# Kernel optimization log

Hardware: AMD Instinct MI355X
Metric: run time of the kernel (lower is better)

Reference implementation:

```python
import math
import jax, jax.numpy as jnp
import numpy as np


def _conv(x, w, b, stride, pad):
    y = jax.lax.conv_general_dilated(x, w, (stride, stride), [(pad, pad), (pad, pad)],
                                     dimension_numbers=('NCHW', 'OIHW', 'NCHW'))
    return y + b[None, :, None, None]


def _deconv(x, w, b):
    y = jax.lax.conv_transpose(x, w, (2, 2), 'SAME', dimension_numbers=('NCHW', 'HWIO', 'NCHW'))
    return y + b[None, :, None, None]


def _res_stack(h, w1, b1, w2, b2):
    for i in range(w1.shape[0]):  # small fixed num_residual_layers
        r = _conv(jax.nn.relu(h), w1[i], b1[i], 1, 1)
        r = _conv(jax.nn.relu(r), w2[i], b2[i], 1, 0)
        h = h + r
    return jax.nn.relu(h)


def _gcn_edges(x, w, b, src, dst):
    n = x.shape[0]
    xl = x @ w
    deg = 1.0 + jax.ops.segment_sum(jnp.ones_like(dst, dtype=xl.dtype), dst, num_segments=n)
    dinv = jax.lax.rsqrt(deg)
    coef = (dinv[src] * dinv[dst])[:, None]
    agg = jax.ops.segment_sum(xl[src] * coef, dst, num_segments=n)
    return agg + xl / deg[:, None] + b


def setup_inputs() -> dict:
    key = jax.random.key(0)
    ks = jax.random.split(key, 40)
    B, C, H, D, E, Hg, R, L, hid = 256, 3, 64, 256, 16, 64, 32, 2, 128
    f = H // 4
    flat = hid * f * f  # 32768

    def n(k, shape, s=0.02):
        return jax.random.normal(k, shape, jnp.float32) * s

    i = jnp.arange(B - 1)
    src = jnp.concatenate([i, i + 1])
    dst = jnp.concatenate([i + 1, i])
    inp = {
        'x': jax.random.normal(ks[0], (B, C, H, H), jnp.float32),
        'eps': jax.random.normal(ks[1], (B, D), jnp.float32),
        'edge_index': jnp.stack([src, dst]).astype(jnp.int32),
        'enc_conv1_w': n(ks[2], (hid // 2, C, 4, 4)), 'enc_conv1_b': n(ks[3], (hid // 2,)),
        'enc_conv2_w': n(ks[4], (hid, hid // 2, 4, 4)), 'enc_conv2_b': n(ks[5], (hid,)),
        'enc_conv3_w': n(ks[6], (hid, hid, 3, 3)), 'enc_conv3_b': n(ks[7], (hid,)),
        'enc_res_w1': n(ks[8], (L, R, hid, 3, 3)), 'enc_res_b1': n(ks[9], (L, R)),
        'enc_res_w2': n(ks[10], (L, hid, R, 1, 1)), 'enc_res_b2': n(ks[11], (L, hid)),
        'fc_mu_w': n(ks[12], (flat, D)), 'fc_mu_b': n(ks[13], (D,)),
        'fc_logvar_w': n(ks[14], (flat, D)), 'fc_logvar_b': n(ks[15], (D,)),
        'dec_fc_w': n(ks[16], (D, flat)), 'dec_fc_b': n(ks[17], (flat,)),
        'dec_res_w1': n(ks[18], (L, R, hid, 3, 3)), 'dec_res_b1': n(ks[19], (L, R)),
        'dec_res_w2': n(ks[20], (L, hid, R, 1, 1)), 'dec_res_b2': n(ks[21], (L, hid)),
        'dec_ct1_w': n(ks[22], (4, 4, hid, hid // 2)), 'dec_ct1_b': n(ks[23], (hid // 2,)),
        'dec_ct2_w': n(ks[24], (4, 4, hid // 2, C)), 'dec_ct2_b': n(ks[25], (C,)),
        'inst_w': n(ks[26], (2, D, D), 0.05), 'inst_b': n(ks[27], (2, D), 0.02),
        'dim_adj_logits': jax.random.normal(ks[28], (D, D), jnp.float32),
        'dim_embeddings': jax.random.normal(ks[29], (D, E), jnp.float32),
        'dg1_w': n(ks[30], (E, Hg), 0.2), 'dg1_b': n(ks[31], (Hg,), 0.02),
        'dg2_w': n(ks[32], (Hg, 1), 0.2), 'dg2_b': n(ks[33], (1,), 0.02),
    }
    return inp


def reference(x, eps, edge_index, enc_conv1_w, enc_conv1_b, enc_conv2_w, enc_conv2_b,
              enc_conv3_w, enc_conv3_b, enc_res_w1, enc_res_b1, enc_res_w2, enc_res_b2,
              fc_mu_w, fc_mu_b, fc_logvar_w, fc_logvar_b, dec_fc_w, dec_fc_b,
              dec_res_w1, dec_res_b1, dec_res_w2, dec_res_b2,
              dec_ct1_w, dec_ct1_b, dec_ct2_w, dec_ct2_b,
              inst_w, inst_b, dim_adj_logits, dim_embeddings, dg1_w, dg1_b, dg2_w, dg2_b):
    B = x.shape[0]
    D = dim_adj_logits.shape[0]
    # ---- encode ----
    h = jax.nn.relu(_conv(x, enc_conv1_w, enc_conv1_b, 2, 1))
    h = jax.nn.relu(_conv(h, enc_conv2_w, enc_conv2_b, 2, 1))
    h = _conv(h, enc_conv3_w, enc_conv3_b, 1, 1)
    h = _res_stack(h, enc_res_w1, enc_res_b1, enc_res_w2, enc_res_b2)
    flat = h.reshape(B, -1)
    mu = flat @ fc_mu_w + fc_mu_b
    logvar = flat @ fc_logvar_w + fc_logvar_b
    sigma = jnp.exp(0.5 * logvar)
    # ---- instance GNN over chain tree ----
    src, dst = edge_index[0], edge_index[1]
    v = mu
    for i in range(inst_w.shape[0]):
        v = jax.nn.relu(_gcn_edges(v, inst_w[i], inst_b[i], src, dst))
    v_inst = v
    # ---- dim GNN: thresholded dense adjacency, dense GCN (math-identical to edge-list GCNConv) ----
    eye = jnp.eye(D, dtype=x.dtype)
    logits = (dim_adj_logits + dim_adj_logits.T) * (1.0 - eye)
    mask = (jax.nn.sigmoid(logits) > 0.5).astype(x.dtype) * (1.0 - eye)
    mask = jnp.where(mask.sum() > 0, mask, 1.0 - eye)  # fallback: complete graph
    a_hat = mask + eye
    dinv = jax.lax.rsqrt(a_hat.sum(1))
    norm_adj = a_hat * dinv[:, None] * dinv[None, :]
    xd = jax.nn.relu(norm_adj @ (dim_embeddings @ dg1_w) + dg1_b)
    dim_importance = (norm_adj @ (xd @ dg2_w) + dg2_b)[:, 0]
    # ---- reparameterize + decode ----
    vv = v_inst * dim_importance[None, :]
    z = mu + sigma * (eps * vv)
    hd = (z @ dec_fc_w + dec_fc_b).reshape(B, enc_conv3_w.shape[0], x.shape[2] // 4, x.shape[3] // 4)
    hd = _res_stack(hd, dec_res_w1, dec_res_b1, dec_res_w2, dec_res_b2)
    hd = jax.nn.relu(_deconv(hd, dec_ct1_w, dec_ct1_b))
    recon = _deconv(hd, dec_ct2_w, dec_ct2_b)
    # ---- ELBO ----
    log_px_z = -jnp.sum((recon - x) ** 2)
    prior = -0.5 * jnp.sum(z ** 2 + math.log(2 * math.pi))
    entropy = 0.5 * jnp.sum(1.0 + jnp.log(sigma ** 2 + 1e-8))
    elbo = log_px_z + prior + entropy
    lv = jnp.log(sigma ** 2 + 1e-8)
    kl_per_dim = -0.5 * (1.0 + lv - mu ** 2 - jnp.exp(lv))
    num_active_dims = jnp.sum(kl_per_dim.mean(0) > 0.01)
    return recon, elbo, num_active_dims, dim_importance, v_inst
```

## Files before the change

### kernel.cpp

```cpp
#include <hip/hip_runtime.h>
#include <math.h>

#define OUT_ELBO  3145728
#define OUT_NACT  3145729
#define OUT_IMP   3145730
#define OUT_VINST 3145986

__device__ __forceinline__ float relu_(float v){ return fmaxf(v, 0.f); }

__device__ __forceinline__ unsigned short f2bf(float f){
  unsigned int u = __float_as_uint(f);
  unsigned int r = (u + 0x7FFFu + ((u>>16)&1u)) >> 16;
  return (unsigned short)r;
}

typedef __attribute__((ext_vector_type(8))) short short8;
typedef __attribute__((ext_vector_type(4))) float f32x4;

__global__ __launch_bounds__(512) void k_conv1(const float* __restrict__ in,
    const float* __restrict__ w, const float* __restrict__ bias, float* __restrict__ out){
  __shared__ float li[13068];
  __shared__ float lw[1536];
  int cohalf = blockIdx.x & 1;
  int n      = blockIdx.x >> 1;
  int co0 = cohalf*32;
  int tid = threadIdx.x;
  for (int i=tid; i<13068; i+=512) li[i] = 0.f;
  __syncthreads();
  const float* ip = in + (size_t)n*12288;
  for (int i=tid; i<12288; i+=512){
    int ci = i >> 12, rem = i & 4095;
    int yy = rem >> 6, xx = rem & 63;
    li[ci*4356 + (yy+1)*66 + xx+1] = ip[i];
  }
  for (int i=tid; i<1536; i+=512){
    int t = i >> 5, c = i & 31;
    lw[i] = w[(co0+c)*48 + t];
  }
  __syncthreads();
  int x = tid & 31, y8 = tid >> 5;
  #pragma unroll
  for (int cc=0; cc<4; cc++){
    float acc[2][8];
    #pragma unroll
    for (int q=0;q<2;q++)
      #pragma unroll
      for (int c=0;c<8;c++) acc[q][c]=0.f;
    #pragma unroll
    for (int ci=0; ci<3; ci++){
      int cb = ci*4356;
      #pragma unroll
      for (int ky=0; ky<4; ky++){
        float v[2][4];
        #pragma unroll
        for (int q=0;q<2;q++){
          int y = y8 + 16*q;
          int rb = cb + (2*y+ky)*66 + 2*x;
          v[q][0]=li[rb]; v[q][1]=li[rb+1]; v[q][2]=li[rb+2]; v[q][3]=li[rb+3];
        }
        float wv[4][8];
        #pragma unroll
        for (int kx=0;kx<4;kx++){
          int wb = ((ci*4+ky)*4+kx)*32 + cc*8;
          #pragma unroll
          for (int c=0;c<8;c++) wv[kx][c] = lw[wb+c];
        }
        #pragma unroll
        for (int q=0;q<2;q++)
          #pragma unroll
          for (int kx=0;kx<4;kx++)
            #pragma unroll
            for (int c=0;c<8;c++)
              acc[q][c] += v[q][kx]*wv[kx][c];
      }
    }
    #pragma unroll
    for (int c=0;c<8;c++){
      int co = co0 + cc*8 + c;
      float bv = bias[co];
      #pragma unroll
      for (int q=0;q<2;q++){
        int y = y8 + 16*q;
        out[(((size_t)n*64+co)*32 + y)*32 + x] = relu_(acc[q][c] + bv);
      }
    }
  }
}

__global__ __launch_bounds__(256) void k_wt2(const float* __restrict__ w,
    unsigned short* __restrict__ Wt){
  int idx = blockIdx.x*256 + threadIdx.x;
  int ci = idx & 63;
  int r = idx >> 6;
  int t = r >> 7, co = r & 127;
  Wt[idx] = f2bf(w[((co*64 + ci)<<4) + t]);
}

__global__ __launch_bounds__(256) void k_at2(const float* __restrict__ in,
    unsigned short* __restrict__ At){
  __shared__ unsigned int l[256*33];
  int n = blockIdx.x, tid = threadIdx.x;
  const float* ip = in + (size_t)n*65536;
  unsigned short* Ab = At + (size_t)n*1156*64;
  for (int c=0;c<4;c++){
    __syncthreads();
    int pxg = c*256 + tid;
    for (int j=0;j<64;j+=2){
      float a = ip[j*1024 + pxg];
      float b = ip[(j+1)*1024 + pxg];
      l[tid*33 + (j>>1)] = (unsigned int)f2bf(a) | ((unsigned int)f2bf(b)<<16);
    }
    __syncthreads();
    #pragma unroll
    for (int it=0; it<8; it++){
      int u = it*256 + tid;
      int pxl = u >> 3, seg = u & 7;
      int pxg2 = c*256 + pxl;
      int y = pxg2 >> 5, x = pxg2 & 31;
      int pp = (y+1)*34 + (x+1);
      uint4 v;
      v.x = l[pxl*33 + seg*4 + 0];
      v.y = l[pxl*33 + seg*4 + 1];
      v.z = l[pxl*33 + seg*4 + 2];
      v.w = l[pxl*33 + seg*4 + 3];
      *(uint4*)(Ab + pp*64 + seg*8) = v;
    }
  }
  uint4 z; z.x=0; z.y=0; z.z=0; z.w=0;
  for (int it=0; it<5; it++){
    int u = it*256 + tid;
    if (u >= 1056) break;
    int h = u >> 3, seg = u & 7;
    int pp;
    if (h < 34) pp = h;
    else if (h < 68) pp = 1122 + (h-34);
    else { int s = h-68; pp = (1 + (s>>1))*34 + (s&1)*33; }
    *(uint4*)(Ab + pp*64 + seg*8) = z;
  }
}

__global__ __launch_bounds__(256) void k_c2mfma(const unsigned short* __restrict__ At,
    const unsigned short* __restrict__ Wt, const float* __restrict__ bias,
    float* __restrict__ out){
  int b = blockIdx.x;
  int wsw = (b & 7)*32 + (b >> 3);
  int half = wsw & 1;
  int n    = wsw >> 1;
  int tid = threadIdx.x;
  int wid = tid >> 6, lane = tid & 63;
  int wn = wid & 1, wm = wid >> 1;
  int lrow = lane & 15, lkb = lane >> 4;
  f32x4 acc[4][4];
  #pragma unroll
  for (int i=0;i<4;i++)
    #pragma unroll
    for (int j=0;j<4;j++){ acc[i][j].x=0.f; acc[i][j].y=0.f; acc[i][j].z=0.f; acc[i][j].w=0.f; }
  const unsigned short* Ab = At + (size_t)n*1156*64;
  int mbase = half*128 + wm*64;
  #pragma unroll
  for (int t=0; t<16; t++){
    int ky = t >> 2, kx = t & 3;
    #pragma unroll
    for (int kc=0; kc<2; kc++){
      int k0 = kc*32 + lkb*8;
      short8 a[4], b2[4];
      #pragma unroll
      for (int i=0;i<4;i++){
        int m = mbase + i*16 + lrow;
        int y = m >> 4, x = m & 15;
        int pp = (2*y+ky)*34 + (2*x+kx);
        a[i] = *(const short8*)(Ab + pp*64 + k0);
      }
      #pragma unroll
      for (int j=0;j<4;j++){
        int co = wn*64 + j*16 + lrow;
        b2[j] = *(const short8*)(Wt + (t*128 + co)*64 + k0);
      }
      #pragma unroll
      for (int i=0;i<4;i++)
        #pragma unroll
        for (int j=0;j<4;j++)
          acc[i][j] = __builtin_amdgcn_mfma_f32_16x16x32_bf16(a[i], b2[j], acc[i][j], 0,0,0);
    }
  }
  #pragma unroll
  for (int j=0;j<4;j++){
    int co = wn*64 + j*16 + lrow;
    float bv = bias[co];
    #pragma unroll
    for (int i=0;i<4;i++){
      int px0 = mbase + i*16 + lkb*4;
      f32x4 v = acc[i][j];
      v.x = relu_(v.x + bv); v.y = relu_(v.y + bv);
      v.z = relu_(v.z + bv); v.w = relu_(v.w + bv);
      *(f32x4*)(out + ((size_t)n*128+co)*256 + px0) = v;
    }
  }
}

__global__ __launch_bounds__(256) void k_wt(const float* __restrict__ w,
    unsigned short* __restrict__ Wt, int Co){
  int idx = blockIdx.x*256 + threadIdx.x;
  int tot = Co*128*9;
  if (idx >= tot) return;
  int ci = idx & 127;
  int r = idx >> 7;
  int t = r / Co, co = r - t*Co;
  Wt[idx] = f2bf(w[(co*128 + ci)*9 + t]);
}

__global__ __launch_bounds__(256) void k_wt1(const float* __restrict__ w,
    unsigned short* __restrict__ Wt){
  int idx = blockIdx.x*256 + threadIdx.x;
  int ci = idx & 127;
  int r = idx >> 7;
  int t = r >> 6, co = r & 63;
  Wt[idx] = f2bf(w[t*8192 + ci*64 + co]);
}

__global__ __launch_bounds__(256) void k_at(const float* __restrict__ in,
    unsigned short* __restrict__ At, int relu){
  __shared__ unsigned int l[256*67];
  int n = blockIdx.x, tid = threadIdx.x;
  for (int j=0;j<128;j+=2){
    float a = in[(n*128+j  )*256 + tid];
    float b = in[(n*128+j+1)*256 + tid];
    if (relu){ a = relu_(a); b = relu_(b); }
    l[tid*67 + (j>>1)] = (unsigned int)f2bf(a) | ((unsigned int)f2bf(b)<<16);
  }
  __syncthreads();
  unsigned short* Ab = At + (size_t)n*324*128;
  #pragma unroll
  for (int it=0; it<16; it++){
    int u = it*256 + tid;
    int px = u >> 4, seg = u & 15;
    int y = px >> 4, x = px & 15;
    int pp = (y+1)*18 + (x+1);
    uint4 v;
    v.x = l[px*67 + seg*4 + 0];
    v.y = l[px*67 + seg*4 + 1];
    v.z = l[px*67 + seg*4 + 2];
    v.w = l[px*67 + seg*4 + 3];
    *(uint4*)(Ab + pp*128 + seg*8) = v;
  }
  uint4 z; z.x=0; z.y=0; z.z=0; z.w=0;
  for (int it=0; it<5; it++){
    int u = it*256 + tid;
    if (u >= 1088) break;
    int h = u >> 4, seg = u & 15;
    int pp;
    if (h < 18) pp = h;
    else if (h < 36) pp = 306 + (h-18);
    else { int s = h-36; pp = 18 + (s>>1)*18 + (s&1)*17; }
    *(uint4*)(Ab + pp*128 + seg*8) = z;
  }
}

template<int CO>
__global__ __launch_bounds__(512) void k_c3mfma(const unsigned short* __restrict__ At,
    const unsigned short* __restrict__ Wt, const float* __restrict__ bias,
    float* __restrict__ out){
  constexpr int WNW = (CO==128) ? 2 : 1;
  constexpr int WMW = 8/WNW;
  constexpr int MT  = 16/WMW;
  constexpr int NT  = (CO/16)/WNW;
  __shared__ short8 lA[16][324];
  int n = blockIdx.x;
  int tid = threadIdx.x;
  const short8* src = (const short8*)(At + (size_t)n*324*128);
  #pragma unroll
  for (int it=0; it<11; it++){
    int u = it*512 + tid;
    if (u < 5184) lA[u & 15][u >> 4] = src[u];
  }
  __syncthreads();
  int wid = tid >> 6, lane = tid & 63;
  int wn = wid % WNW, wm = wid / WNW;
  int lrow = lane & 15, lkb = lane >> 4;
  f32x4 acc[MT][NT];
  #pragma unroll
  for (int i=0;i<MT;i++)
    #pragma unroll
    for (int j=0;j<NT;j++){ acc[i][j].x=0.f; acc[i][j].y=0.f; acc[i][j].z=0.f; acc[i][j].w=0.f; }
  for (int t=0; t<9; t++){
    int ky = t/3, kx = t - 3*(t/3);
    #pragma unroll
    for (int kc=0; kc<4; kc++){
      int ch = kc*4 + lkb;
      int k0 = kc*32 + lkb*8;
      short8 a[MT], b[NT];
      #pragma unroll
      for (int i=0;i<MT;i++){
        int m = wm*(MT*16) + i*16 + lrow;
        int y = m >> 4, x = m & 15;
        int pp = (y+ky)*18 + (x+kx);
        a[i] = lA[ch][pp];
      }
      #pragma unroll
      for (int j=0;j<NT;j++){
        int co = wn*(NT*16) + j*16 + lrow;
        b[j] = *(const short8*)(Wt + (t*CO + co)*128 + k0);
      }
      #pragma unroll
      for (int i=0;i<MT;i++)
        #pragma unroll
        for (int j=0;j<NT;j++)
          acc[i][j] = __builtin_amdgcn_mfma_f32_16x16x32_bf16(a[i], b[j], acc[i][j], 0,0,0);
    }
  }
  #pragma unroll
  for (int j=0;j<NT;j++){
    int co = wn*(NT*16) + j*16 + lrow;
    float bv = bias[co];
    #pragma unroll
    for (int i=0;i<MT;i++){
      int px0 = wm*(MT*16) + i*16 + lkb*4;
      f32x4 v = acc[i][j];
      v.x += bv; v.y += bv; v.z += bv; v.w += bv;
      *(f32x4*)(out + ((size_t)n*CO+co)*256 + px0) = v;
    }
  }
}

__global__ __launch_bounds__(512) void k_dc1mfma(const unsigned short* __restrict__ At,
    const unsigned short* __restrict__ Wt, const float* __restrict__ bias,
    float* __restrict__ out){
  __shared__ short8 lA[16][324];
  int b = blockIdx.x;
  int wsw = (b & 7)*64 + (b >> 3);
  int half = wsw & 1;
  int n    = wsw >> 1;
  int tid = threadIdx.x;
  const short8* src = (const short8*)(At + (size_t)n*324*128);
  #pragma unroll
  for (int it=0; it<11; it++){
    int u = it*512 + tid;
    if (u < 5184) lA[u & 15][u >> 4] = src[u];
  }
  __syncthreads();
  int wid = tid >> 6, lane = tid & 63;
  int cls = half*2 + (wid >> 2);
  int wm  = wid & 3;
  int p_y = cls >> 1, p_x = cls & 1;
  int lrow = lane & 15, lkb = lane >> 4;
  f32x4 acc[4][4];
  #pragma unroll
  for (int i=0;i<4;i++)
    #pragma unroll
    for (int j=0;j<4;j++){ acc[i][j].x=0.f; acc[i][j].y=0.f; acc[i][j].z=0.f; acc[i][j].w=0.f; }
  #pragma unroll
  for (int kc=0; kc<16; kc++){
    int tapi = kc >> 2;
    int a = tapi >> 1, bb = tapi & 1;
    int ch = (kc & 3)*4 + lkb;
    int k0 = (kc & 3)*32 + lkb*8;
    int t = (p_y + 2*a)*4 + (p_x + 2*bb);
    short8 av[4], bv[4];
    #pragma unroll
    for (int i=0;i<4;i++){
      int m = wm*64 + i*16 + lrow;
      int gy = m >> 4, gx = m & 15;
      int pp = (gy + p_y + a)*18 + (gx + p_x + bb);
      av[i] = lA[ch][pp];
    }
    #pragma unroll
    for (int j=0;j<4;j++){
      int co = j*16 + lrow;
      bv[j] = *(const short8*)(Wt + (t*64 + co)*128 + k0);
    }
    #pragma unroll
    for (int i=0;i<4;i++)
      #pragma unroll
      for (int j=0;j<4;j++)
        acc[i][j] = __builtin_amdgcn_mfma_f32_16x16x32_bf16(av[i], bv[j], acc[i][j], 0,0,0);
  }
  #pragma unroll
  for (int j=0;j<4;j++){
    int co = j*16 + lrow;
    float bvf = bias[co];
    float* op = out + (((size_t)n*64 + co)*4 + cls)*256;
    #pragma unroll
    for (int i=0;i<4;i++){
      int m0 = wm*64 + i*16 + lkb*4;
      f32x4 v = acc[i][j];
      v.x = relu_(v.x + bvf); v.y = relu_(v.y + bvf);
      v.z = relu_(v.z + bvf); v.w = relu_(v.w + bvf);
      *(f32x4*)(op + m0) = v;
    }
  }
}

__global__ __launch_bounds__(256) void k_res1x1(const float* __restrict__ r,
    const float* __restrict__ w, const float* __restrict__ bias, float* __restrict__ h){
  int tid = threadIdx.x, n = blockIdx.x;
  float rv[32];
  #pragma unroll
  for (int ci=0;ci<32;ci++) rv[ci] = relu_(r[(n*32+ci)*256 + tid]);
  for (int co=0;co<128;co++){
    float a = bias[co];
    const float* wp = w + co*32;
    #pragma unroll
    for (int ci=0;ci<32;ci++) a += rv[ci]*wp[ci];
    h[(n*128+co)*256 + tid] += a;
  }
}

__global__ __launch_bounds__(256) void k_f2b(const float* __restrict__ in,
    unsigned short* __restrict__ out, int n4, int relu){
  int i = blockIdx.x*256 + threadIdx.x;
  if (i >= n4) return;
  float4 v = ((const float4*)in)[i];
  if (relu){ v.x=relu_(v.x); v.y=relu_(v.y); v.z=relu_(v.z); v.w=relu_(v.w); }
  uint2 o;
  o.x = (unsigned int)f2bf(v.x) | ((unsigned int)f2bf(v.y)<<16);
  o.y = (unsigned int)f2bf(v.z) | ((unsigned int)f2bf(v.w)<<16);
  ((uint2*)out)[i] = o;
}

__global__ __launch_bounds__(256) void k_wtd(const float* __restrict__ w,
    unsigned short* __restrict__ Wt){
  __shared__ unsigned int l[256*65];
  int j0 = blockIdx.x*256;
  int tid = threadIdx.x;
  for (int half=0; half<2; half++){
    __syncthreads();
    int kb = half*128;
    for (int k=0;k<128;k+=2){
      float a = w[(size_t)(kb+k  )*32768 + j0 + tid];
      float b = w[(size_t)(kb+k+1)*32768 + j0 + tid];
      l[tid*65 + (k>>1)] = (unsigned int)f2bf(a) | ((unsigned int)f2bf(b)<<16);
    }
    __syncthreads();
    #pragma unroll
    for (int it=0; it<16; it++){
      int u = it*256 + tid;
      int j = u >> 4, seg = u & 15;
      uint4 v;
      v.x = l[j*65 + seg*4 + 0];
      v.y = l[j*65 + seg*4 + 1];
      v.z = l[j*65 + seg*4 + 2];
      v.w = l[j*65 + seg*4 + 3];
      *(uint4*)(Wt + (size_t)(j0+j)*256 + kb + seg*8) = v;
    }
  }
}

__global__ __launch_bounds__(256) void k_wtfc(const float* __restrict__ w,
    unsigned short* __restrict__ Wt, int dbase){
  __shared__ unsigned int l[256*65];
  int k0 = blockIdx.x*256;
  int tid = threadIdx.x;
  for (int half=0; half<2; half++){
    __syncthreads();
    int kb = half*128;
    for (int k=0;k<128;k+=2){
      float a = w[(size_t)(k0+kb+k  )*256 + tid];
      float b = w[(size_t)(k0+kb+k+1)*256 + tid];
      l[tid*65 + (k>>1)] = (unsigned int)f2bf(a) | ((unsigned int)f2bf(b)<<16);
    }
    __syncthreads();
    #pragma unroll
    for (int it=0; it<16; it++){
      int u = it*256 + tid;
      int d = u >> 4, seg = u & 15;
      uint4 v;
      v.x = l[d*65 + seg*4 + 0];
      v.y = l[d*65 + seg*4 + 1];
      v.z = l[d*65 + seg*4 + 2];
      v.w = l[d*65 + seg*4 + 3];
      *(uint4*)(Wt + (size_t)(dbase+d)*32768 + k0 + kb + seg*8) = v;
    }
  }
}

__global__ __launch_bounds__(512) void k_dfmfma(const unsigned short* __restrict__ zb,
    const unsigned short* __restrict__ Wt, const float* __restrict__ bias,
    float* __restrict__ hd){
  int jbase = blockIdx.x*128;
  int tid = threadIdx.x;
  int wid = tid >> 6, lane = tid & 63;
  int wn = wid & 1, wm = wid >> 1;
  int lrow = lane & 15, lkb = lane >> 4;
  f32x4 acc[4][4];
  #pragma unroll
  for (int i=0;i<4;i++)
    #pragma unroll
    for (int j=0;j<4;j++){ acc[i][j].x=0.f; acc[i][j].y=0.f; acc[i][j].z=0.f; acc[i][j].w=0.f; }
  #pragma unroll
  for (int kc=0; kc<8; kc++){
    int k0 = kc*32 + lkb*8;
    short8 a[4], b[4];
    #pragma unroll
    for (int i=0;i<4;i++){
      int m = wm*64 + i*16 + lrow;
      a[i] = *(const short8*)(zb + m*256 + k0);
    }
    #pragma unroll
    for (int j=0;j<4;j++){
      int jj = jbase + wn*64 + j*16 + lrow;
      b[j] = *(const short8*)(Wt + (size_t)jj*256 + k0);
    }
    #pragma unroll
    for (int i=0;i<4;i++)
      #pragma unroll
      for (int j=0;j<4;j++)
        acc[i][j] = __builtin_amdgcn_mfma_f32_16x16x32_bf16(a[i], b[j], acc[i][j], 0,0,0);
  }
  #pragma unroll
  for (int j=0;j<4;j++){
    int jj = jbase + wn*64 + j*16 + lrow;
    float bv = bias[jj];
    #pragma unroll
    for (int i=0;i<4;i++){
      int m0 = wm*64 + i*16 + lkb*4;
      f32x4 v = acc[i][j];
      hd[(size_t)(m0  )*32768 + jj] = v.x + bv;
      hd[(size_t)(m0+1)*32768 + jj] = v.y + bv;
      hd[(size_t)(m0+2)*32768 + jj] = v.z + bv;
      hd[(size_t)(m0+3)*32768 + jj] = v.w + bv;
    }
  }
}

__global__ __launch_bounds__(512) void k_efmfma(const unsigned short* __restrict__ Ab,
    const unsigned short* __restrict__ Wt, float* __restrict__ P){
  int ks = blockIdx.x >> 2;
  int ng = blockIdx.x & 3;
  int kchunk = ks*512;
  int tid = threadIdx.x;
  int wid = tid >> 6, lane = tid & 63;
  int wn = wid & 1, wm = wid >> 1;
  int lrow = lane & 15, lkb = lane >> 4;
  f32x4 acc[4][4];
  #pragma unroll
  for (int i=0;i<4;i++)
    #pragma unroll
    for (int j=0;j<4;j++){ acc[i][j].x=0.f; acc[i][j].y=0.f; acc[i][j].z=0.f; acc[i][j].w=0.f; }
  #pragma unroll
  for (int kc=0; kc<16; kc++){
    int k0 = kchunk + kc*32 + lkb*8;
    short8 a[4], b[4];
    #pragma unroll
    for (int i=0;i<4;i++){
      int m = wm*64 + i*16 + lrow;
      a[i] = *(const short8*)(Ab + (size_t)m*32768 + k0);
    }
    #pragma unroll
    for (int j=0;j<4;j++){
      int n = ng*128 + wn*64 + j*16 + lrow;
      b[j] = *(const short8*)(Wt + (size_t)n*32768 + k0);
    }
    #pragma unroll
    for (int i=0;i<4;i++)
      #pragma unroll
      for (int j=0;j<4;j++)
        acc[i][j] = __builtin_amdgcn_mfma_f32_16x16x32_bf16(a[i], b[j], acc[i][j], 0,0,0);
  }
  #pragma unroll
  for (int j=0;j<4;j++){
    int n = ng*128 + wn*64 + j*16 + lrow;
    #pragma unroll
    for (int i=0;i<4;i++){
      int m0 = wm*64 + i*16 + lkb*4;
      f32x4 v = acc[i][j];
      P[((size_t)ks*256 + m0  )*512 + n] = v.x;
      P[((size_t)ks*256 + m0+1)*512 + n] = v.y;
      P[((size_t)ks*256 + m0+2)*512 + n] = v.z;
      P[((size_t)ks*256 + m0+3)*512 + n] = v.w;
    }
  }
}

__global__ __launch_bounds__(256) void k_efred(const float* __restrict__ P,
    const float* __restrict__ bmu, const float* __restrict__ blv,
    float* __restrict__ mu, float* __restrict__ lv){
  int idx = blockIdx.x*256 + threadIdx.x;
  int m = idx >> 8, d = idx & 255;
  float sm=0.f, sl=0.f;
  for (int ks=0; ks<64; ks++){
    size_t base = ((size_t)ks*256 + m)*512;
    sm += P[base + d];
    sl += P[base + 256 + d];
  }
  mu[idx] = sm + bmu[d];
  lv[idx] = sl + blv[d];
}

__global__ void k_deg(const int* __restrict__ ei, int ne, float* __restrict__ deg,
                      float* __restrict__ dinv){
  int n = threadIdx.x;
  const int* dst = ei + ne;
  int c = 1;
  for (int e=0;e<ne;e++) c += (dst[e]==n) ? 1 : 0;
  deg[n]  = (float)c;
  dinv[n] = rsqrtf((float)c);
}

__global__ __launch_bounds__(256) void k_zero(float* __restrict__ p, int n){
  int i = blockIdx.x*256 + threadIdx.x;
  if (i<n) p[i]=0.f;
}

__global__ __launch_bounds__(256) void k_gemm256(const float* __restrict__ v,
    const float* __restrict__ w, float* __restrict__ xl){
  __shared__ float vl[256];
  int n = blockIdx.x, tid = threadIdx.x;
  vl[tid] = v[(n<<8)+tid];
  __syncthreads();
  float a=0.f;
  for (int k=0;k<256;k++) a += vl[k]*w[(k<<8)+tid];
  xl[(n<<8)+tid]=a;
}

__global__ __launch_bounds__(256) void k_edge(const int* __restrict__ ei, int ne,
    const float* __restrict__ xl, const float* __restrict__ dinv, float* __restrict__ agg){
  int e = blockIdx.x, d = threadIdx.x;
  int s = ei[e], t = ei[ne+e];
  float c = dinv[s]*dinv[t];
  atomicAdd(&agg[(t<<8)+d], xl[(s<<8)+d]*c);
}

__global__ __launch_bounds__(256) void k_gcnout(const float* __restrict__ agg,
    const float* __restrict__ xl, const float* __restrict__ deg, const float* __restrict__ bias,
    float* __restrict__ vout, float* __restrict__ vout2){
  int idx = blockIdx.x*256 + threadIdx.x;
  int n = idx>>8, d = idx&255;
  float o = relu_(agg[idx] + xl[idx]/deg[n] + bias[d]);
  vout[idx]=o;
  if (vout2) vout2[idx]=o;
}

__global__ __launch_bounds__(256) void k_y1(const float* __restrict__ emb,
    const float* __restrict__ w, float* __restrict__ y1){
  int idx = blockIdx.x*256+threadIdx.x;
  int i = idx>>6, h = idx&63;
  float a=0.f;
  #pragma unroll
  for (int k=0;k<16;k++) a += emb[i*16+k]*w[k*64+h];
  y1[idx]=a;
}

__global__ __launch_bounds__(256) void k_mask(const float* __restrict__ L,
    float* __restrict__ mask, float* __restrict__ rowcnt){
  __shared__ float red[256];
  int i = blockIdx.x, j = threadIdx.x;
  float m = (i!=j && (L[(i<<8)+j] + L[(j<<8)+i] > 0.f)) ? 1.f : 0.f;
  mask[(i<<8)+j]=m;
  red[j]=m; __syncthreads();
  for (int s=128;s>0;s>>=1){ if(j<s) red[j]+=red[j+s]; __syncthreads(); }
  if (j==0) rowcnt[i]=red[0];
}

__global__ __launch_bounds__(256) void k_dimdeg(const float* __restrict__ rowcnt,
    float* __restrict__ ddinv, float* __restrict__ fbflag){
  __shared__ float red[256];
  int i = threadIdx.x;
  red[i]=rowcnt[i]; __syncthreads();
  for (int s=128;s>0;s>>=1){ if(i<s) red[i]+=red[i+s]; __syncthreads(); }
  float fb = (red[0] > 0.f) ? 0.f : 1.f;
  float degi = 1.f + (fb>0.5f ? 255.f : rowcnt[i]);
  ddinv[i] = rsqrtf(degi);
  if (i==0) fbflag[0]=fb;
}

__global__ __launch_bounds__(64) void k_xd(const float* __restrict__ mask,
    const float* __restrict__ ddinv, const float* __restrict__ y1,
    const float* __restrict__ b, const float* __restrict__ fbflag, float* __restrict__ xd){
  int i = blockIdx.x, h = threadIdx.x;
  float fb = fbflag[0];
  float dii = ddinv[i];
  float a=0.f;
  for (int j=0;j<256;j++){
    float ah = (j==i) ? 1.f : (fb>0.5f ? 1.f : mask[(i<<8)+j]);
    a += ah*dii*ddinv[j]*y1[(j<<6)+h];
  }
  xd[(i<<6)+h] = relu_(a + b[h]);
}

__global__ __launch_bounds__(256) void k_imp(const float* __restrict__ xd,
    const float* __restrict__ w2, const float* __restrict__ b2,
    const float* __restrict__ mask, const float* __restrict__ ddinv,
    const float* __restrict__ fbflag, float* __restrict__ imp, float* __restrict__ imp_out){
  __shared__ float t[256];
  int i = threadIdx.x;
  float a=0.f;
  #pragma unroll
  for (int h=0;h<64;h++) a += xd[(i<<6)+h]*w2[h];
  t[i]=a; __syncthreads();
  float fb=fbflag[0]; float dii=ddinv[i];
  float s=0.f;
  for (int j=0;j<256;j++){
    float ah = (j==i) ? 1.f : (fb>0.5f ? 1.f : mask[(i<<8)+j]);
    s += ah*dii*ddinv[j]*t[j];
  }
  float r = s + b2[0];
  imp[i]=r; imp_out[i]=r;
}

__global__ __launch_bounds__(256) void k_reparam(const float* __restrict__ mu,
    const float* __restrict__ lv, const float* __restrict__ eps,
    const float* __restrict__ v2, const float* __restrict__ imp, float* __restrict__ z){
  int idx = blockIdx.x*256+threadIdx.x;
  int d = idx&255;
  float s = expf(0.5f*lv[idx]);
  z[idx] = mu[idx] + s*(eps[idx]*(v2[idx]*imp[d]));
}

__global__ __launch_bounds__(512) void k_deconv2(const float* __restrict__ in,
    const float* __restrict__ w, const float* __restrict__ bias, float* __restrict__ out){
  __shared__ float tile[4096];
  int p_x = blockIdx.x & 1;
  int n   = blockIdx.x >> 1;
  int tid = threadIdx.x;
  int xi = tid & 31, yb = tid >> 5;
  int x = 2*xi + p_x;
  int ix0 = xi + p_x - 1, ix1 = xi + p_x;
  bool okx0 = (unsigned)ix0 < 32u, okx1 = (unsigned)ix1 < 32u;
  int r0 = 2*yb - 1;
  int su[8];
  #pragma unroll
  for (int t=0;t<8;t++){
    int u = t*512 + tid;
    int px = u & 1023;
    int r = px >> 5, c = px & 31;
    su[t] = (((r&1)<<1)|(c&1))*256 + ((r>>1)<<4) + (c>>1);
  }
  float acc[4][3];
  #pragma unroll
  for (int r=0;r<4;r++)
    #pragma unroll
    for (int c=0;c<3;c++) acc[r][c]=0.f;
  for (int c0=0; c0<64; c0+=4){
    __syncthreads();
    #pragma unroll
    for (int t=0;t<8;t++){
      int u = t*512 + tid;
      int cil = u >> 10;
      const float* ip = in + ((size_t)n*64 + c0 + cil)*1024;
      tile[u] = ip[su[t]];
    }
    __syncthreads();
    #pragma unroll
    for (int cil=0; cil<4; cil++){
      const float* tl = tile + cil*1024;
      float tv[4][2];
      #pragma unroll
      for (int rr=0; rr<4; rr++){
        int row = r0 + rr;
        bool okr = (unsigned)row < 32u;
        tv[rr][0] = (okr && okx0) ? tl[row*32+ix0] : 0.f;
        tv[rr][1] = (okr && okx1) ? tl[row*32+ix1] : 0.f;
      }
      const float* wp = w + (c0+cil)*3;
      #pragma unroll
      for (int r=0;r<4;r++){
        int py = r & 1;
        int rA = (r==0)?0:((r==3)?2:1);
        int rB = (r==0)?1:((r==3)?3:2);
        #pragma unroll
        for (int b=0;b<2;b++){
          int kx = p_x + 2*b;
          const float* w0 = wp + (py*4+kx)*192;
          const float* w1 = wp + ((py+2)*4+kx)*192;
          float vA = tv[rA][b], vB = tv[rB][b];
          #pragma unroll
          for (int c=0;c<3;c++){
            acc[r][c] += vA * w0[c];
            acc[r][c] += vB * w1[c];
          }
        }
      }
    }
  }
  #pragma unroll
  for (int c=0;c<3;c++){
    float bv = bias[c];
    #pragma unroll
    for (int r=0;r<4;r++){
      int y = 4*yb + r;
      out[(((size_t)n*3+c)*64 + y)*64 + x] = acc[r][c] + bv;
    }
  }
}

__global__ __launch_bounds__(256) void k_sse(const float* __restrict__ recon,
    const float* __restrict__ x, float* __restrict__ part){
  __shared__ float red[256];
  int tid = threadIdx.x;
  float a=0.f;
  for (int i = blockIdx.x*256+tid; i<3145728; i += gridDim.x*256){
    float d = recon[i]-x[i]; a += d*d;
  }
  red[tid]=a; __syncthreads();
  for (int s=128;s>0;s>>=1){ if(tid<s) red[tid]+=red[tid+s]; __syncthreads(); }
  if (tid==0) part[blockIdx.x]=red[0];
}

__global__ __launch_bounds__(256) void k_stats(const float* __restrict__ mu,
    const float* __restrict__ lv, const float* __restrict__ z,
    float* __restrict__ z2part, float* __restrict__ entpart, float* __restrict__ klflag){
  __shared__ float r1[256], r2[256], r3[256];
  int d = blockIdx.x, n = threadIdx.x;
  int idx = (n<<8) + d;
  float m = mu[idx], l = lv[idx], zz = z[idx];
  float s2e = expf(l) + 1e-8f;
  float leps = logf(s2e);
  r1[n] = zz*zz;
  r2[n] = 1.f + leps;
  r3[n] = -0.5f*(1.f + leps - m*m - s2e);
  __syncthreads();
  for (int s=128;s>0;s>>=1){
    if (n<s){ r1[n]+=r1[n+s]; r2[n]+=r2[n+s]; r3[n]+=r3[n+s]; }
    __syncthreads();
  }
  if (n==0){
    z2part[d]=r1[0]; entpart[d]=r2[0];
    klflag[d] = (r3[0]*(1.f/256.f) > 0.01f) ? 1.f : 0.f;
  }
}

__global__ __launch_bounds__(256) void k_final(const float* __restrict__ ssepart,
    const float* __restrict__ z2part, const float* __restrict__ entpart,
    const float* __restrict__ klflag, float* __restrict__ out){
  __shared__ float red[256];
  int tid = threadIdx.x;
  float s=0.f;
  for (int i=tid;i<1024;i+=256) s += ssepart[i];
  red[tid]=s; __syncthreads();
  for (int st=128;st>0;st>>=1){ if(tid<st) red[tid]+=red[tid+st]; __syncthreads(); }
  float sse = red[0]; __syncthreads();
  red[tid]=z2part[tid]; __syncthreads();
  for (int st=128;st>0;st>>=1){ if(tid<st) red[tid]+=red[tid+st]; __syncthreads(); }
  float z2 = red[0]; __syncthreads();
  red[tid]=entpart[tid]; __syncthreads();
  for (int st=128;st>0;st>>=1){ if(tid<st) red[tid]+=red[tid+st]; __syncthreads(); }
  float ent = red[0]; __syncthreads();
  red[tid]=klflag[tid]; __syncthreads();
  for (int st=128;st>0;st>>=1){ if(tid<st) red[tid]+=red[tid+st]; __syncthreads(); }
  if (tid==0){
    float logpxz  = -sse;
    float prior   = -0.5f*(z2 + 65536.f*1.8378770664093453f);
    float entropy = 0.5f*ent;
    out[OUT_ELBO] = logpxz + prior + entropy;
    out[OUT_NACT] = red[0];
  }
}

extern "C" void kernel_launch(void* const* d_in, const int* in_sizes, int n_in,
                              void* d_out, int out_size, void* d_ws, size_t ws_size,
                              hipStream_t stream){
  const float* x    = (const float*)d_in[0];
  const float* eps  = (const float*)d_in[1];
  const int*   ei   = (const int*)d_in[2];
  const float* c1w  = (const float*)d_in[3];
  const float* c1b  = (const float*)d_in[4];
  const float* c2w  = (const float*)d_in[5];
  const float* c2b  = (const float*)d_in[6];
  const float* c3w  = (const float*)d_in[7];
  const float* c3b  = (const float*)d_in[8];
  const float* erw1 = (const float*)d_in[9];
  const float* erb1 = (const float*)d_in[10];
  const float* erw2 = (const float*)d_in[11];
  const float* erb2 = (const float*)d_in[12];
  const float* fmw  = (const float*)d_in[13];
  const float* fmb  = (const float*)d_in[14];
  const float* flw  = (const float*)d_in[15];
  const float* flb  = (const float*)d_in[16];
  const float* dfw  = (const float*)d_in[17];
  const float* dfb  = (const float*)d_in[18];
  const float* drw1 = (const float*)d_in[19];
  const float* drb1 = (const float*)d_in[20];
  const float* drw2 = (const float*)d_in[21];
  const float* drb2 = (const float*)d_in[22];
  const float* t1w  = (const float*)d_in[23];
  const float* t1b  = (const float*)d_in[24];
  const float* t2w  = (const float*)d_in[25];
  const float* t2b  = (const float*)d_in[26];
  const float* iw   = (const float*)d_in[27];
  const float* ib   = (const float*)d_in[28];
  const float* Lg   = (const float*)d_in[29];
  const float* emb  = (const float*)d_in[30];
  const float* g1w  = (const float*)d_in[31];
  const float* g1b  = (const float*)d_in[32];
  const float* g2w  = (const float*)d_in[33];
  const float* g2b  = (const float*)d_in[34];
  float* out = (float*)d_out;
  float* ws  = (float*)d_ws;
  int ne = in_sizes[2] / 2;

  float* A  = ws;
  float* Bb = ws + 16777216;
  float* Cc = Bb + 8388608;
  float* Rr = A;
  float* P  = A + 2097152;
  unsigned short* At = (unsigned short*)(A + 10485760);
  unsigned short* Ab = (unsigned short*)(A + 10485760);
  unsigned short* Wt = (unsigned short*)(A + 15794176);
  unsigned short* At2 = (unsigned short*)Cc;
  unsigned short* Wt2 = (unsigned short*)(Cc + 5242880);
  unsigned short* Wtd = (unsigned short*)Cc;
  unsigned short* Atd = (unsigned short*)Cc;
  unsigned short* Wt1 = (unsigned short*)(Cc + 5308416);
  unsigned short* Wtfc = (unsigned short*)Bb;
  float* S  = Cc + 8388608;
  float* mu     = S; S += 65536;
  float* lv     = S; S += 65536;
  float* v1     = S; S += 65536;
  float* v2     = S; S += 65536;
  float* xl     = S; S += 65536;
  float* agg    = S; S += 65536;
  float* zz     = S; S += 65536;
  float* mask   = S; S += 65536;
  float* y1     = S; S += 16384;
  float* xd     = S; S += 16384;
  float* zbf    = S; S += 32768;
  float* deg    = S; S += 256;
  float* dinvb  = S; S += 256;
  float* rowcnt = S; S += 256;
  float* ddinv  = S; S += 256;
  float* fbflag = S; S += 256;
  float* impv   = S; S += 256;
  float* ssep   = S; S += 1024;
  float* z2p    = S; S += 256;
  float* entp   = S; S += 256;
  float* klf    = S; S += 256;
  unsigned short* zb = (unsigned short*)zbf;

  k_conv1<<<512,512,0,stream>>>(x, c1w, c1b, A);
  k_wt2<<<512,256,0,stream>>>(c2w, Wt2);
  for (int pass=0; pass<2; pass++){
    size_t n0 = (size_t)pass*128;
    k_at2<<<128,256,0,stream>>>(A + n0*65536, At2);
    k_c2mfma<<<256,256,0,stream>>>(At2, Wt2, c2b, Bb + n0*32768);
  }
  k_wt<<<576,256,0,stream>>>(c3w, Wt, 128);
  k_at<<<256,256,0,stream>>>(Bb, At, 0);
  k_c3mfma<128><<<256,512,0,stream>>>(At, Wt, c3b, Cc);
  k_wt<<<144,256,0,stream>>>(erw1, Wt, 32);
  k_at<<<256,256,0,stream>>>(Cc, At, 1);
  k_c3mfma<32><<<256,512,0,stream>>>(At, Wt, erb1, Rr);
  k_res1x1<<<256,256,0,stream>>>(Rr, erw2, erb2, Cc);
  k_wt<<<144,256,0,stream>>>(erw1+36864, Wt, 32);
  k_at<<<256,256,0,stream>>>(Cc, At, 1);
  k_c3mfma<32><<<256,512,0,stream>>>(At, Wt, erb1+32, Rr);
  k_res1x1<<<256,256,0,stream>>>(Rr, erw2+4096, erb2+128, Cc);
  k_f2b<<<8192,256,0,stream>>>(Cc, Ab, 2097152, 1);
  k_wtfc<<<128,256,0,stream>>>(fmw, Wtfc, 0);
  k_wtfc<<<128,256,0,stream>>>(flw, Wtfc, 256);
  k_efmfma<<<256,512,0,stream>>>(Ab, Wtfc, P);
  k_efred<<<256,256,0,stream>>>(P, fmb, flb, mu, lv);

  k_deg<<<1,256,0,stream>>>(ei, ne, deg, dinvb);
  k_gemm256<<<256,256,0,stream>>>(mu, iw, xl);
  k_zero<<<256,256,0,stream>>>(agg, 65536);
  k_edge<<<ne,256,0,stream>>>(ei, ne, xl, dinvb, agg);
  k_gcnout<<<256,256,0,stream>>>(agg, xl, deg, ib, v1, nullptr);
  k_gemm256<<<256,256,0,stream>>>(v1, iw+65536, xl);
  k_zero<<<256,256,0,stream>>>(agg, 65536);
  k_edge<<<ne,256,0,stream>>>(ei, ne, xl, dinvb, agg);
  k_gcnout<<<256,256,0,stream>>>(agg, xl, deg, ib+256, v2, out + OUT_VINST);

  k_y1<<<64,256,0,stream>>>(emb, g1w, y1);
  k_mask<<<256,256,0,stream>>>(Lg, mask, rowcnt);
  k_dimdeg<<<1,256,0,stream>>>(rowcnt, ddinv, fbflag);
  k_xd<<<256,64,0,stream>>>(mask, ddinv, y1, g1b, fbflag, xd);
  k_imp<<<1,256,0,stream>>>(xd, g2w, g2b, mask, ddinv, fbflag, impv, out + OUT_IMP);

  k_reparam<<<256,256,0,stream>>>(mu, lv, eps, v2, impv, zz);
  k_f2b<<<64,256,0,stream>>>(zz, zb, 16384, 0);
  k_wtd<<<128,256,0,stream>>>(dfw, Wtd);
  k_dfmfma<<<256,512,0,stream>>>(zb, Wtd, dfb, Bb);
  k_wt<<<144,256,0,stream>>>(drw1, Wt, 32);
  k_at<<<256,256,0,stream>>>(Bb, At, 1);
  k_c3mfma<32><<<256,512,0,stream>>>(At, Wt, drb1, Rr);
  k_res1x1<<<256,256,0,stream>>>(Rr, drw2, drb2, Bb);
  k_wt<<<144,256,0,stream>>>(drw1+36864, Wt, 32);
  k_at<<<256,256,0,stream>>>(Bb, At, 1);
  k_c3mfma<32><<<256,512,0,stream>>>(At, Wt, drb1+32, Rr);
  k_res1x1<<<256,256,0,stream>>>(Rr, drw2+4096, erb2+128 == erb2+128 ? drb2+128 : drb2+128, Bb);
  k_wt1<<<512,256,0,stream>>>(t1w, Wt1);
  k_at<<<256,256,0,stream>>>(Bb, Atd, 1);
  k_dc1mfma<<<512,512,0,stream>>>(Atd, Wt1, t1b, A);
  k_deconv2<<<512,512,0,stream>>>(A, t2w, t2b, out);

  k_sse<<<1024,256,0,stream>>>(out, x, ssep);
  k_stats<<<256,256,0,stream>>>(mu, lv, zz, z2p, entp, klf);
  k_final<<<1,256,0,stream>>>(ssep, z2p, entp, klf, out);
}
```

Baseline: 899.2 us.

## Restructure final deconv: one block per image, 3x3 neighborhood reuse, double-buffered tiles

The final 64->3 transposed conv now uses one 1024-thread block per image instead of two 512-thread blocks split by output column parity. Each thread owns one input pixel, loads its 3x3 neighborhood once per channel, and computes all four output phases from it. Input channels are staged in 8-channel groups through double-buffered shared memory with register prefetch, and outputs are written as float2. This removes the duplicated input staging and reloads of the earlier parity split, at the cost of fewer blocks and larger shared memory per block.

```diff
diff --git a/kernel.cpp b/kernel.cpp
--- a/kernel.cpp
+++ b/kernel.cpp
@@ -706,80 +706,82 @@
   z[idx] = mu[idx] + s*(eps[idx]*(v2[idx]*imp[d]));
 }
 
-__global__ __launch_bounds__(512) void k_deconv2(const float* __restrict__ in,
+__global__ __launch_bounds__(1024) void k_deconv2(const float* __restrict__ in,
     const float* __restrict__ w, const float* __restrict__ bias, float* __restrict__ out){
-  __shared__ float tile[4096];
-  int p_x = blockIdx.x & 1;
-  int n   = blockIdx.x >> 1;
-  int tid = threadIdx.x;
-  int xi = tid & 31, yb = tid >> 5;
-  int x = 2*xi + p_x;
-  int ix0 = xi + p_x - 1, ix1 = xi + p_x;
-  bool okx0 = (unsigned)ix0 < 32u, okx1 = (unsigned)ix1 < 32u;
-  int r0 = 2*yb - 1;
-  int su[8];
-  #pragma unroll
-  for (int t=0;t<8;t++){
-    int u = t*512 + tid;
-    int px = u & 1023;
-    int r = px >> 5, c = px & 31;
-    su[t] = (((r&1)<<1)|(c&1))*256 + ((r>>1)<<4) + (c>>1);
-  }
-  float acc[4][3];
-  #pragma unroll
-  for (int r=0;r<4;r++)
-    #pragma unroll
-    for (int c=0;c<3;c++) acc[r][c]=0.f;
-  for (int c0=0; c0<64; c0+=4){
-    __syncthreads();
-    #pragma unroll
-    for (int t=0;t<8;t++){
-      int u = t*512 + tid;
-      int cil = u >> 10;
-      const float* ip = in + ((size_t)n*64 + c0 + cil)*1024;
-      tile[u] = ip[su[t]];
-    }
-    __syncthreads();
-    #pragma unroll
-    for (int cil=0; cil<4; cil++){
-      const float* tl = tile + cil*1024;
-      float tv[4][2];
-      #pragma unroll
-      for (int rr=0; rr<4; rr++){
-        int row = r0 + rr;
-        bool okr = (unsigned)row < 32u;
-        tv[rr][0] = (okr && okx0) ? tl[row*32+ix0] : 0.f;
-        tv[rr][1] = (okr && okx1) ? tl[row*32+ix1] : 0.f;
-      }
-      const float* wp = w + (c0+cil)*3;
-      #pragma unroll
-      for (int r=0;r<4;r++){
-        int py = r & 1;
-        int rA = (r==0)?0:((r==3)?2:1);
-        int rB = (r==0)?1:((r==3)?3:2);
+  __shared__ float tile[2][8192];
+  int n = blockIdx.x;
+  int tid = threadIdx.x;
+  int p = tid & 31, q = tid >> 5;
+  bool okc0 = p >= 1, okc2 = p < 31;
+  bool okr0 = q >= 1, okr2 = q < 31;
+  int r = tid >> 5, c = tid & 31;
+  int su = (((r&1)<<1)|(c&1))*256 + ((r>>1)<<4) + (c>>1);
+  const float* ip0 = in + (size_t)n*65536;
+  float acc[2][2][3];
+  #pragma unroll
+  for (int py=0;py<2;py++)
+    #pragma unroll
+    for (int px=0;px<2;px++)
+      #pragma unroll
+      for (int cc=0;cc<3;cc++) acc[py][px][cc]=0.f;
+  float rg[8];
+  #pragma unroll
+  for (int t=0;t<8;t++) rg[t] = ip0[t*1024 + su];
+  #pragma unroll
+  for (int t=0;t<8;t++) tile[0][t*1024 + tid] = rg[t];
+  __syncthreads();
+  for (int s=0; s<8; s++){
+    int nxt = s+1;
+    if (nxt < 8){
+      #pragma unroll
+      for (int t=0;t<8;t++) rg[t] = ip0[(nxt*8+t)*1024 + su];
+    }
+    const float* tb = tile[s&1];
+    #pragma unroll
+    for (int cil=0; cil<8; cil++){
+      int ci = s*8 + cil;
+      const float* tl = tb + cil*1024;
+      float tv[3][3];
+      tv[0][0] = (okr0 && okc0) ? tl[(q-1)*32 + (p-1)] : 0.f;
+      tv[0][1] = okr0           ? tl[(q-1)*32 +  p   ] : 0.f;
+      tv[0][2] = (okr0 && okc2) ? tl[(q-1)*32 + (p+1)] : 0.f;
+      tv[1][0] = okc0           ? tl[ q   *32 + (p-1)] : 0.f;
+      tv[1][1] =                  tl[ q   *32 +  p   ];
+      tv[1][2] = okc2           ? tl[ q   *32 + (p+1)] : 0.f;
+      tv[2][0] = (okr2 && okc0) ? tl[(q+1)*32 + (p-1)] : 0.f;
+      tv[2][1] = okr2           ? tl[(q+1)*32 +  p   ] : 0.f;
+      tv[2][2] = (okr2 && okc2) ? tl[(q+1)*32 + (p+1)] : 0.f;
+      const float* wp = w + ci*3;
+      #pragma unroll
+      for (int py=0;py<2;py++){
         #pragma unroll
-        for (int b=0;b<2;b++){
-          int kx = p_x + 2*b;
-          const float* w0 = wp + (py*4+kx)*192;
-          const float* w1 = wp + ((py+2)*4+kx)*192;
-          float vA = tv[rA][b], vB = tv[rB][b];
+        for (int px=0;px<2;px++){
+          const float* wAA = wp + ( py   *4 + px  )*192;
+          const float* wAB = wp + ( py   *4 + px+2)*192;
+          const float* wBA = wp + ((py+2)*4 + px  )*192;
+          const float* wBB = wp + ((py+2)*4 + px+2)*192;
+          float vAA = tv[py][px],   vAB = tv[py][px+1];
+          float vBA = tv[py+1][px], vBB = tv[py+1][px+1];
           #pragma unroll
-          for (int c=0;c<3;c++){
-            acc[r][c] += vA * w0[c];
-            acc[r][c] += vB * w1[c];
+          for (int cc=0;cc<3;cc++){
+            acc[py][px][cc] += vAA*wAA[cc] + vAB*wAB[cc] + vBA*wBA[cc] + vBB*wBB[cc];
           }
         }
       }
     }
-  }
-  #pragma unroll
-  for (int c=0;c<3;c++){
-    float bv = bias[c];
-    #pragma unroll
-    for (int r=0;r<4;r++){
-      int y = 4*yb + r;
-      out[(((size_t)n*3+c)*64 + y)*64 + x] = acc[r][c] + bv;
-    }
+    if (nxt < 8){
+      #pragma unroll
+      for (int t=0;t<8;t++) tile[nxt&1][t*1024 + tid] = rg[t];
+    }
+    __syncthreads();
+  }
+  #pragma unroll
+  for (int cc=0;cc<3;cc++){
+    float bv = bias[cc];
+    float2 v0; v0.x = acc[0][0][cc] + bv; v0.y = acc[0][1][cc] + bv;
+    float2 v1; v1.x = acc[1][0][cc] + bv; v1.y = acc[1][1][cc] + bv;
+    *(float2*)(out + (((size_t)n*3+cc)*64 + 2*q  )*64 + 2*p) = v0;
+    *(float2*)(out + (((size_t)n*3+cc)*64 + 2*q+1)*64 + 2*p) = v1;
   }
 }
 
@@ -977,11 +979,11 @@
   k_wt<<<144,256,0,stream>>>(drw1+36864, Wt, 32);
   k_at<<<256,256,0,stream>>>(Bb, At, 1);
   k_c3mfma<32><<<256,512,0,stream>>>(At, Wt, drb1+32, Rr);
-  k_res1x1<<<256,256,0,stream>>>(Rr, drw2+4096, erb2+128 == erb2+128 ? drb2+128 : drb2+128, Bb);
+  k_res1x1<<<256,256,0,stream>>>(Rr, drw2+4096, drb2+128, Bb);
   k_wt1<<<512,256,0,stream>>>(t1w, Wt1);
   k_at<<<256,256,0,stream>>>(Bb, Atd, 1);
   k_dc1mfma<<<512,512,0,stream>>>(Atd, Wt1, t1b, A);
-  k_deconv2<<<512,512,0,stream>>>(A, t2w, t2b, out);
+  k_deconv2<<<256,1024,0,stream>>>(A, t2w, t2b, out);
 
   k_sse<<<1024,256,0,stream>>>(out, x, ssep);
   k_stats<<<256,256,0,stream>>>(mu, lv, zz, z2p, entp, klf);
```

New measurement: 915.0 us. Within noise of the previous version (+1.8%).
